# Optimization experiments

Hardware: AMD Instinct MI355X
Metric: run time of the kernel (lower is better)

## Reference

```python
import jax, jax.numpy as jnp
import numpy as np

BSZ, D = 256, 512
LOGIT_SCALE = 1.0


def setup_inputs() -> dict:
    key = jax.random.key(0)
    k1, k2, k3 = jax.random.split(key, 3)
    x = jax.random.normal(k1, (BSZ, D), dtype=jnp.float32)
    y = jax.random.normal(k2, (BSZ, D), dtype=jnp.float32)
    z = jax.random.normal(k3, (BSZ, D), dtype=jnp.float32)
    return {"x": x, "y": y, "z": z}


def _logits_n_squared(anchor, a, b, shift):
    # torch recursion: products[i*bsz + r] = a[r] * roll(b, i)[r] = a[r] * b[(r - i) % bsz]
    bsz = anchor.shape[0]
    P = a[None, :, :] * b[shift]              # (i, r, d) = (bsz, bsz, d)
    logits = jnp.einsum('ad,ird->air', anchor, P)  # (a, i, r)
    return LOGIT_SCALE * logits.reshape(bsz, bsz * bsz)


def _cross_entropy_diag(logits):
    bsz = logits.shape[0]
    lp = jax.nn.log_softmax(logits, axis=-1)
    idx = jnp.arange(bsz)
    return -jnp.mean(lp[idx, idx])


def reference(x, y, z):
    bsz = x.shape[0]
    r = jnp.arange(bsz)
    shift = (r[None, :] - r[:, None]) % bsz   # (i, r): index into b after roll by i
    reps = [x, y, z]
    losses = []
    for i in range(3):
        anchor = reps[i]
        non_anchor = [reps[j] for j in range(3) if j != i]
        logits = _logits_n_squared(anchor, non_anchor[0], non_anchor[1], shift)
        losses.append(_cross_entropy_diag(logits))
    return sum(losses) / 3.0
```

## Files before the change

### kernel.cpp

```cpp
#include <hip/hip_runtime.h>

#define DIM 512
#define BK 32

typedef unsigned int uint;
typedef unsigned short ushort;
typedef __attribute__((ext_vector_type(8))) short short8;
typedef __attribute__((ext_vector_type(4))) float f32x4;

__device__ __forceinline__ uint pack_bf16(float a, float b) {
    union { float f; uint u; } ua, ub;
    ua.f = a; ub.f = b;
    uint x0 = ua.u + 0x8000u;
    uint x1 = ub.u + 0x8000u;
    return __builtin_amdgcn_perm(x1, x0, 0x07060302);
}

__global__ void __launch_bounds__(512, 4)
gemm_fused(const float* __restrict__ x, const float* __restrict__ y,
           const float* __restrict__ z,
           float* __restrict__ rowM, float* __restrict__ rowS,
           float* __restrict__ colM, float* __restrict__ colS,
           float* __restrict__ diag, uint* __restrict__ counter) {
    __shared__ __align__(16) float xs[DIM];
    __shared__ __align__(16) ushort As[128 * BK];
    __shared__ __align__(16) ushort Bs[256 * BK];
    __shared__ float redA[128 * 4];
    __shared__ float rowMaxS[128];
    __shared__ float redB[256 * 2];
    __shared__ float colMaxS[256];
    __shared__ float dred[8];

    const int tid = threadIdx.x;
    const int a   = blockIdx.x >> 1;
    const int rt  = blockIdx.x & 1;

    if (blockIdx.x == 0 && tid == 0) *counter = 0u;

    xs[tid] = x[a * DIM + tid];

    const int lane = tid & 63;
    const int wave = tid >> 6;
    const int quad = lane >> 4;
    const int ln15 = lane & 15;
    const int wr = wave >> 2;
    const int wc = wave & 3;

    if (rt == 0) {
        float p = xs[tid] * y[a * DIM + tid] * z[a * DIM + tid];
        #pragma unroll
        for (int m = 1; m < 64; m <<= 1) p += __shfl_xor(p, m, 64);
        if (lane == 0) dred[wave] = p;
        __syncthreads();
        if (tid == 0) {
            float s = 0.f;
            #pragma unroll
            for (int w2 = 0; w2 < 8; ++w2) s += dred[w2];
            diag[a] = s;
        }
    }

    f32x4 acc[4][4];
    #pragma unroll
    for (int i = 0; i < 4; ++i)
        #pragma unroll
        for (int j = 0; j < 4; ++j)
            acc[i][j] = (f32x4){0.f, 0.f, 0.f, 0.f};

    const int fA = tid * 8;
    const int rA = fA >> 5;
    const int kA = fA & 31;
    const float* yrow = y + (rt * 128 + rA) * DIM + kA;

    const int fB = tid * 16;
    const int sB = fB >> 5;
    const int kB = fB & 31;
    const float* zrow = z + sB * DIM + kB;

    for (int kt = 0; kt < DIM / BK; ++kt) {
        const int k0 = kt * BK;
        __syncthreads();
        {
            float4 y0 = *(const float4*)(yrow + k0);
            float4 y1 = *(const float4*)(yrow + k0 + 4);
            float4 x0 = *(const float4*)(xs + k0 + kA);
            float4 x1 = *(const float4*)(xs + k0 + kA + 4);
            uint4 o;
            o.x = pack_bf16(y0.x * x0.x, y0.y * x0.y);
            o.y = pack_bf16(y0.z * x0.z, y0.w * x0.w);
            o.z = pack_bf16(y1.x * x1.x, y1.y * x1.y);
            o.w = pack_bf16(y1.z * x1.z, y1.w * x1.w);
            *(uint4*)(As + fA) = o;
        }
        {
            float4 z0 = *(const float4*)(zrow + k0);
            float4 z1 = *(const float4*)(zrow + k0 + 4);
            float4 z2 = *(const float4*)(zrow + k0 + 8);
            float4 z3 = *(const float4*)(zrow + k0 + 12);
            uint4 o0, o1;
            o0.x = pack_bf16(z0.x, z0.y);
            o0.y = pack_bf16(z0.z, z0.w);
            o0.z = pack_bf16(z1.x, z1.y);
            o0.w = pack_bf16(z1.z, z1.w);
            o1.x = pack_bf16(z2.x, z2.y);
            o1.y = pack_bf16(z2.z, z2.w);
            o1.z = pack_bf16(z3.x, z3.y);
            o1.w = pack_bf16(z3.z, z3.w);
            *(uint4*)(Bs + fB) = o0;
            *(uint4*)(Bs + fB + 8) = o1;
        }
        __syncthreads();
        short8 af[4], bfr[4];
        #pragma unroll
        for (int i = 0; i < 4; ++i)
            af[i] = *(const short8*)(As + (wr * 64 + i * 16 + ln15) * BK + quad * 8);
        #pragma unroll
        for (int j = 0; j < 4; ++j)
            bfr[j] = *(const short8*)(Bs + (wc * 64 + j * 16 + ln15) * BK + quad * 8);
        #pragma unroll
        for (int i = 0; i < 4; ++i)
            #pragma unroll
            for (int j = 0; j < 4; ++j)
                acc[i][j] = __builtin_amdgcn_mfma_f32_16x16x32_bf16(af[i], bfr[j], acc[i][j], 0, 0, 0);
    }
    __syncthreads();

    #pragma unroll
    for (int i = 0; i < 4; ++i) {
        #pragma unroll
        for (int reg = 0; reg < 4; ++reg) {
            float m = fmaxf(fmaxf(acc[i][0][reg], acc[i][1][reg]),
                            fmaxf(acc[i][2][reg], acc[i][3][reg]));
            #pragma unroll
            for (int d = 1; d < 16; d <<= 1) m = fmaxf(m, __shfl_xor(m, d, 64));
            if (ln15 == 0) redA[(wr * 64 + i * 16 + quad * 4 + reg) * 4 + wc] = m;
        }
    }
    __syncthreads();
    if (tid < 128) {
        float m = fmaxf(fmaxf(redA[tid * 4 + 0], redA[tid * 4 + 1]),
                        fmaxf(redA[tid * 4 + 2], redA[tid * 4 + 3]));
        rowMaxS[tid] = m;
    }
    __syncthreads();
    #pragma unroll
    for (int i = 0; i < 4; ++i) {
        #pragma unroll
        for (int reg = 0; reg < 4; ++reg) {
            int r = wr * 64 + i * 16 + quad * 4 + reg;
            float rm = rowMaxS[r];
            float s = __expf(acc[i][0][reg] - rm) + __expf(acc[i][1][reg] - rm)
                    + __expf(acc[i][2][reg] - rm) + __expf(acc[i][3][reg] - rm);
            #pragma unroll
            for (int d = 1; d < 16; d <<= 1) s += __shfl_xor(s, d, 64);
            if (ln15 == 0) redA[r * 4 + wc] = s;
        }
    }
    __syncthreads();
    if (tid < 128) {
        float s = redA[tid * 4 + 0] + redA[tid * 4 + 1] + redA[tid * 4 + 2] + redA[tid * 4 + 3];
        int rg = rt * 128 + tid;
        rowM[a * 256 + rg] = rowMaxS[tid];
        rowS[a * 256 + rg] = s;
    }

    #pragma unroll
    for (int j = 0; j < 4; ++j) {
        float m = -3.4e38f;
        #pragma unroll
        for (int i = 0; i < 4; ++i)
            #pragma unroll
            for (int reg = 0; reg < 4; ++reg)
                m = fmaxf(m, acc[i][j][reg]);
        m = fmaxf(m, __shfl_xor(m, 16, 64));
        m = fmaxf(m, __shfl_xor(m, 32, 64));
        if (quad == 0) redB[(wc * 64 + j * 16 + ln15) * 2 + wr] = m;
    }
    __syncthreads();
    if (tid < 256) colMaxS[tid] = fmaxf(redB[tid * 2], redB[tid * 2 + 1]);
    __syncthreads();
    #pragma unroll
    for (int j = 0; j < 4; ++j) {
        int n = wc * 64 + j * 16 + ln15;
        float cm = colMaxS[n];
        float s = 0.f;
        #pragma unroll
        for (int i = 0; i < 4; ++i)
            #pragma unroll
            for (int reg = 0; reg < 4; ++reg)
                s += __expf(acc[i][j][reg] - cm);
        s += __shfl_xor(s, 16, 64);
        s += __shfl_xor(s, 32, 64);
        if (quad == 0) redB[n * 2 + wr] = s;
    }
    __syncthreads();
    if (tid < 256) {
        float s = redB[tid * 2] + redB[tid * 2 + 1];
        colM[(a * 256 + tid) * 2 + rt] = colMaxS[tid];
        colS[(a * 256 + tid) * 2 + rt] = s;
    }
}

__device__ __forceinline__ float blk_max(float v, float* sm) {
    #pragma unroll
    for (int d = 1; d < 64; d <<= 1) v = fmaxf(v, __shfl_xor(v, d, 64));
    __syncthreads();
    if ((threadIdx.x & 63) == 0) sm[threadIdx.x >> 6] = v;
    __syncthreads();
    return fmaxf(fmaxf(sm[0], sm[1]), fmaxf(sm[2], sm[3]));
}
__device__ __forceinline__ float blk_sum(float v, float* sm) {
    #pragma unroll
    for (int d = 1; d < 64; d <<= 1) v += __shfl_xor(v, d, 64);
    __syncthreads();
    if ((threadIdx.x & 63) == 0) sm[threadIdx.x >> 6] = v;
    __syncthreads();
    return sm[0] + sm[1] + sm[2] + sm[3];
}

__global__ void combine_final(const float* __restrict__ rowM, const float* __restrict__ rowS,
                              const float* __restrict__ colM, const float* __restrict__ colS,
                              const float* __restrict__ diag,
                              float* __restrict__ m123, uint* __restrict__ counter,
                              float* __restrict__ out) {
    __shared__ float sm[4];
    __shared__ uint isLast;
    int b = blockIdx.x, t = threadIdx.x;
    float m = rowM[b * 256 + t], s = rowS[b * 256 + t];
    float M = blk_max(m, sm);
    float S = blk_sum(s * __expf(m - M), sm);
    float M1 = M + __logf(S);
    m = rowM[t * 256 + b]; s = rowS[t * 256 + b];
    M = blk_max(m, sm);
    S = blk_sum(s * __expf(m - M), sm);
    float M2 = M + __logf(S);
    float am = colM[(t * 256 + b) * 2 + 0], av = colS[(t * 256 + b) * 2 + 0];
    float bm = colM[(t * 256 + b) * 2 + 1], bv = colS[(t * 256 + b) * 2 + 1];
    m = fmaxf(am, bm);
    s = av * __expf(am - m) + bv * __expf(bm - m);
    M = blk_max(m, sm);
    S = blk_sum(s * __expf(m - M), sm);
    float M3 = M + __logf(S);
    if (t == 0) {
        m123[b] = M1 + M2 + M3;
        __threadfence();
        isLast = (atomicAdd(counter, 1u) == 255u) ? 1u : 0u;
    }
    __syncthreads();
    if (isLast) {
        __threadfence();
        const volatile float* vm = (const volatile float*)m123;
        const volatile float* vd = (const volatile float*)diag;
        float S1 = blk_sum(vm[t], sm);
        float S2 = blk_sum(vd[t], sm);
        if (t == 0) out[0] = S1 / 768.0f - S2 / 256.0f;
    }
}

extern "C" void kernel_launch(void* const* d_in, const int* in_sizes, int n_in,
                              void* d_out, int out_size, void* d_ws, size_t ws_size,
                              hipStream_t stream) {
    const float* x = (const float*)d_in[0];
    const float* y = (const float*)d_in[1];
    const float* z = (const float*)d_in[2];
    char* w = (char*)d_ws;
    float* rowM = (float*)(w);
    float* rowS = (float*)(w + 262144);
    float* colM = (float*)(w + 524288);
    float* colS = (float*)(w + 1048576);
    float* diag = (float*)(w + 1572864);
    float* m123 = (float*)(w + 1573888);
    uint*  counter = (uint*)(w + 1574912);
    float* out  = (float*)d_out;

    gemm_fused<<<512, 512, 0, stream>>>(x, y, z, rowM, rowS, colM, colS, diag, counter);
    combine_final<<<256, 256, 0, stream>>>(rowM, rowS, colM, colS, diag, m123, counter, out);
}
```

Baseline: 103.9 us.

## Pre-convert z to bf16 and stream it into LDS via direct global loads

Adds a small kernel that converts z to bf16 once into the workspace. The fused GEMM then loads the B tile straight into LDS with global_load_lds, using a swizzled chunk layout, instead of having every block re-read fp32 z and convert it in registers. It also pads the A tile's LDS row stride to 40 to reduce bank conflicts. The aim is to cut redundant global traffic and conversion ALU work across the 512 blocks, at the cost of an extra kernel launch and workspace offsets that shift.

```diff
diff --git a/kernel.cpp b/kernel.cpp
--- a/kernel.cpp
+++ b/kernel.cpp
@@ -2,6 +2,7 @@
 
 #define DIM 512
 #define BK 32
+#define ASTRIDE 40
 
 typedef unsigned int uint;
 typedef unsigned short ushort;
@@ -16,14 +17,27 @@
     return __builtin_amdgcn_perm(x1, x0, 0x07060302);
 }
 
+__global__ void zconv_kernel(const float* __restrict__ z, ushort* __restrict__ zb) {
+    int t = blockIdx.x * 256 + threadIdx.x;
+    int f = t * 8;
+    float4 a = *(const float4*)(z + f);
+    float4 b = *(const float4*)(z + f + 4);
+    uint4 o;
+    o.x = pack_bf16(a.x, a.y);
+    o.y = pack_bf16(a.z, a.w);
+    o.z = pack_bf16(b.x, b.y);
+    o.w = pack_bf16(b.z, b.w);
+    *(uint4*)(zb + f) = o;
+}
+
 __global__ void __launch_bounds__(512, 4)
 gemm_fused(const float* __restrict__ x, const float* __restrict__ y,
-           const float* __restrict__ z,
+           const ushort* __restrict__ zb, const float* __restrict__ z,
            float* __restrict__ rowM, float* __restrict__ rowS,
            float* __restrict__ colM, float* __restrict__ colS,
            float* __restrict__ diag, uint* __restrict__ counter) {
     __shared__ __align__(16) float xs[DIM];
-    __shared__ __align__(16) ushort As[128 * BK];
+    __shared__ __align__(16) ushort As[128 * ASTRIDE];
     __shared__ __align__(16) ushort Bs[256 * BK];
     __shared__ float redA[128 * 4];
     __shared__ float rowMaxS[128];
@@ -67,19 +81,26 @@
         for (int j = 0; j < 4; ++j)
             acc[i][j] = (f32x4){0.f, 0.f, 0.f, 0.f};
 
-    const int fA = tid * 8;
-    const int rA = fA >> 5;
-    const int kA = fA & 31;
+    const int rA = tid >> 2;
+    const int kA = (tid & 3) * 8;
     const float* yrow = y + (rt * 128 + rA) * DIM + kA;
 
-    const int fB = tid * 16;
-    const int sB = fB >> 5;
-    const int kB = fB & 31;
-    const float* zrow = z + sB * DIM + kB;
+    const int s0 = wave * 128 + lane;
+    const int row0 = s0 >> 2, kc0 = ((s0 & 3) - (row0 >> 1)) & 3;
+    const ushort* gB0 = zb + row0 * DIM + kc0 * 8;
+    const int s1 = s0 + 64;
+    const int row1 = s1 >> 2, kc1 = ((s1 & 3) - (row1 >> 1)) & 3;
+    const ushort* gB1 = zb + row1 * DIM + kc1 * 8;
 
     for (int kt = 0; kt < DIM / BK; ++kt) {
         const int k0 = kt * BK;
         __syncthreads();
+        __builtin_amdgcn_global_load_lds(
+            (const __attribute__((address_space(1))) void*)(gB0 + k0),
+            (__attribute__((address_space(3))) void*)(Bs + wave * 1024), 16, 0, 0);
+        __builtin_amdgcn_global_load_lds(
+            (const __attribute__((address_space(1))) void*)(gB1 + k0),
+            (__attribute__((address_space(3))) void*)(Bs + wave * 1024 + 512), 16, 0, 0);
         {
             float4 y0 = *(const float4*)(yrow + k0);
             float4 y1 = *(const float4*)(yrow + k0 + 4);
@@ -90,33 +111,19 @@
             o.y = pack_bf16(y0.z * x0.z, y0.w * x0.w);
             o.z = pack_bf16(y1.x * x1.x, y1.y * x1.y);
             o.w = pack_bf16(y1.z * x1.z, y1.w * x1.w);
-            *(uint4*)(As + fA) = o;
-        }
-        {
-            float4 z0 = *(const float4*)(zrow + k0);
-            float4 z1 = *(const float4*)(zrow + k0 + 4);
-            float4 z2 = *(const float4*)(zrow + k0 + 8);
-            float4 z3 = *(const float4*)(zrow + k0 + 12);
-            uint4 o0, o1;
-            o0.x = pack_bf16(z0.x, z0.y);
-            o0.y = pack_bf16(z0.z, z0.w);
-            o0.z = pack_bf16(z1.x, z1.y);
-            o0.w = pack_bf16(z1.z, z1.w);
-            o1.x = pack_bf16(z2.x, z2.y);
-            o1.y = pack_bf16(z2.z, z2.w);
-            o1.z = pack_bf16(z3.x, z3.y);
-            o1.w = pack_bf16(z3.z, z3.w);
-            *(uint4*)(Bs + fB) = o0;
-            *(uint4*)(Bs + fB + 8) = o1;
+            *(uint4*)(As + rA * ASTRIDE + kA) = o;
         }
         __syncthreads();
         short8 af[4], bfr[4];
         #pragma unroll
         for (int i = 0; i < 4; ++i)
-            af[i] = *(const short8*)(As + (wr * 64 + i * 16 + ln15) * BK + quad * 8);
-        #pragma unroll
-        for (int j = 0; j < 4; ++j)
-            bfr[j] = *(const short8*)(Bs + (wc * 64 + j * 16 + ln15) * BK + quad * 8);
+            af[i] = *(const short8*)(As + (wr * 64 + i * 16 + ln15) * ASTRIDE + quad * 8);
+        #pragma unroll
+        for (int j = 0; j < 4; ++j) {
+            int row = wc * 64 + j * 16 + ln15;
+            int pos = row * 4 + ((quad + (row >> 1)) & 3);
+            bfr[j] = *(const short8*)(Bs + pos * 8);
+        }
         #pragma unroll
         for (int i = 0; i < 4; ++i)
             #pragma unroll
@@ -264,15 +271,17 @@
     const float* y = (const float*)d_in[1];
     const float* z = (const float*)d_in[2];
     char* w = (char*)d_ws;
-    float* rowM = (float*)(w);
-    float* rowS = (float*)(w + 262144);
-    float* colM = (float*)(w + 524288);
-    float* colS = (float*)(w + 1048576);
-    float* diag = (float*)(w + 1572864);
-    float* m123 = (float*)(w + 1573888);
-    uint*  counter = (uint*)(w + 1574912);
+    ushort* zb  = (ushort*)(w);
+    float* rowM = (float*)(w + 262144);
+    float* rowS = (float*)(w + 524288);
+    float* colM = (float*)(w + 786432);
+    float* colS = (float*)(w + 1310720);
+    float* diag = (float*)(w + 1835008);
+    float* m123 = (float*)(w + 1836032);
+    uint*  counter = (uint*)(w + 1837056);
     float* out  = (float*)d_out;
 
-    gemm_fused<<<512, 512, 0, stream>>>(x, y, z, rowM, rowS, colM, colS, diag, counter);
+    zconv_kernel<<<64, 256, 0, stream>>>(z, zb);
+    gemm_fused<<<512, 512, 0, stream>>>(x, y, zb, z, rowM, rowS, colM, colS, diag, counter);
     combine_final<<<256, 256, 0, stream>>>(rowM, rowS, colM, colS, diag, m123, counter, out);
 }
```

Measured after the change: 101.0 us. 2.8% less time.
